# Kernel optimization log

Hardware: AMD Instinct MI355X
Metric: run time of the kernel (lower is better)

The kernel has to match this reference:

```python
import jax, jax.numpy as jnp
import numpy as np

EPS_BN = 1e-5
K_INTERP = 8
K_NEIGH = 16


def _bn(x, g, b):
    # BatchNorm1d in training mode: batch stats over rows (biased var), eps=1e-5
    m = x.mean(axis=0)
    v = x.var(axis=0)
    return (x - m) * jax.lax.rsqrt(v + EPS_BN) * g + b


def _dist(a, b):
    # a:(B,N,3), b:(B,M,3) -> Euclidean distance (B,N,M), computed via the
    # quadratic expansion (clamped at 0) instead of materializing (B,N,M,3)
    d2 = (jnp.sum(a * a, -1)[:, :, None] + jnp.sum(b * b, -1)[:, None, :]
          - 2.0 * jnp.einsum('bnc,bmc->bnm', a, b))
    return jnp.sqrt(jnp.maximum(d2, 0.0))


def _gather(feats, idx):
    # feats:(B,M,C), idx:(B,N,K) int -> (B,N,K,C)
    return jax.vmap(lambda f, i: f[i])(feats, idx)


def setup_inputs() -> dict:
    key = jax.random.key(0)
    B, N1, N2, DS, DD, DOUT = 4, 4096, 1024, 128, 64, 256
    ks = jax.random.split(key, 20)
    s = 0.02
    inp = {
        'p1': jax.random.uniform(ks[0], (B * N1, 3), jnp.float32),
        'x1': jax.random.normal(ks[1], (B * N1, DD), jnp.float32),
        'o1': (jnp.arange(B, dtype=jnp.int32) + 1) * N1,
        'p2': jax.random.uniform(ks[2], (B * N2, 3), jnp.float32),
        'x2': jax.random.normal(ks[3], (B * N2, DS), jnp.float32),
        'o2': (jnp.arange(B, dtype=jnp.int32) + 1) * N2,
        'batch_size': B,
        # dense_mlp: Linear(DD,DS) + BN
        'W_dense': jax.random.normal(ks[4], (DD, DS), jnp.float32) * s,
        'b_dense': jnp.zeros((DS,), jnp.float32),
        'g_dense': jnp.ones((DS,), jnp.float32),
        'bt_dense': jnp.zeros((DS,), jnp.float32),
        # CrossAttentionPointTransformerLayer (dim=DS, hidden_mult=1)
        'Wq': jax.random.normal(ks[5], (DS, DS), jnp.float32) * s,
        'Wk': jax.random.normal(ks[6], (DS, DS), jnp.float32) * s,
        'Wv': jax.random.normal(ks[7], (DS, DS), jnp.float32) * s,
        'W1': jax.random.normal(ks[8], (DS, DS), jnp.float32) * s,
        'b1': jnp.zeros((DS,), jnp.float32),
        'g1': jnp.ones((DS,), jnp.float32),
        'bt1': jnp.zeros((DS,), jnp.float32),
        'W2': jax.random.normal(ks[9], (DS, DS), jnp.float32) * s,
        'b2': jnp.zeros((DS,), jnp.float32),
        # output mlp: Linear(DS+DD, DOUT) + BN
        'W_out': jax.random.normal(ks[10], (DS + DD, DOUT), jnp.float32) * s,
        'b_out': jnp.zeros((DOUT,), jnp.float32),
        'g_out': jnp.ones((DOUT,), jnp.float32),
        'bt_out': jnp.zeros((DOUT,), jnp.float32),
    }
    return inp


def reference(p1, x1, o1, p2, x2, o2, batch_size,
              W_dense, b_dense, g_dense, bt_dense,
              Wq, Wk, Wv, W1, b1, g1, bt1, W2, b2,
              W_out, b_out, g_out, bt_out):
    B = int(batch_size)
    N1 = p1.shape[0] // B
    N2 = p2.shape[0] // B
    DS = x2.shape[-1]

    # dense_mlp
    x1_dense = jax.nn.relu(_bn(x1 @ W_dense + b_dense, g_dense, bt_dense))  # (B*N1, DS)

    # pointops.interpolation(p2, p1, x2, o2, o1, k=8): inverse-distance kNN interp
    p1b = p1.reshape(B, N1, 3)
    p2b = p2.reshape(B, N2, 3)
    x2b = x2.reshape(B, N2, DS)
    d12 = _dist(p1b, p2b)                       # (B,N1,N2)
    negd, idx = jax.lax.top_k(-d12, K_INTERP)   # k nearest in p2
    dknn = -negd
    recip = 1.0 / (dknn + 1e-8)
    w = recip / recip.sum(-1, keepdims=True)    # (B,N1,8)
    x2_interp = jnp.einsum('bnk,bnkc->bnc', w, _gather(x2b, idx))  # (B,N1,DS)

    # CrossAttentionPointTransformerLayer(x_e=x1_dense, x_r=x_d=x2_interp, pos=p1)
    x_e = x1_dense.reshape(B, N1, DS)
    q = x_e @ Wq
    k = x2_interp @ Wk
    v = x2_interp @ Wv
    rel_dist = _dist(p1b, p1b)                  # (B,N1,N1)
    _, nidx = jax.lax.top_k(-rel_dist, K_NEIGH) # 16 nearest neighbors
    kg = _gather(k, nidx)                        # (B,N1,16,DS)
    vg = _gather(v, nidx)
    xeg = _gather(x_e, nidx)
    qk_rel = q[:, :, None, :] - kg
    v2 = vg + xeg
    h = (qk_rel + xeg).reshape(-1, DS)           # (B*N1*16, DS)
    h = jax.nn.relu(_bn(h @ W1 + b1, g1, bt1))
    sim = (h @ W2 + b2).reshape(B, N1, K_NEIGH, DS)
    attn = jax.nn.softmax(sim, axis=-2)          # over neighbors
    agg = jnp.einsum('bnkc,bnkc->bnc', attn, v2).reshape(B * N1, DS)

    # output mlp
    x = jax.nn.relu(_bn(jnp.concatenate([agg, x1], axis=-1) @ W_out + b_out,
                        g_out, bt_out))
    return (p1, x, o1)
```

## Files before the change

kernel.cpp:

```cpp
#include <hip/hip_runtime.h>
#include <math.h>

#define BB 4
#define NN1 4096
#define NN2 1024
#define DS 128
#define DD 64
#define DOUT 256
#define M1 16384
#define MH 262144
#define KCAT 192
#define KI 8
#define KN 16

#define OUT_P1 49152
#define OUT_X  49152
#define OUT_O1 4243456


static const size_t OFF_HPRE = 0;
static const size_t OFF_WTS  = 16777216;
static const size_t OFF_TMP  = 33554432;
static const size_t OFF_XD   = OFF_TMP  + 2097152;
static const size_t OFF_XI   = OFF_XD   + 2097152;
static const size_t OFF_Q    = OFF_XI   + 2097152;
static const size_t OFF_K    = OFF_Q    + 2097152;
static const size_t OFF_V    = OFF_K    + 2097152;
static const size_t OFF_OUTP = OFF_V    + 2097152;
static const size_t OFF_NIDX = OFF_OUTP + 4194304;
static const size_t OFF_STAT = OFF_NIDX + 262144;
static const size_t OFF_P1Q  = OFF_STAT + 4096;
static const size_t OFF_P2Q  = OFF_P1Q  + 65536;
static const size_t OFF_P1S  = OFF_P2Q  + 16384;
static const size_t OFF_P2S  = OFF_P1S  + 65536;

#define WDH 0
#define WDL 8192
#define WQH 16384
#define WQL 32768
#define WKH 49152
#define WKL 65536
#define WVH 81920
#define WVL 98304
#define W1H 114688
#define W1L 131072
#define W2H 147456
#define W2L 163840
#define WOH 180224
#define WOL 229376

typedef __attribute__((ext_vector_type(8))) short short8;
typedef __attribute__((ext_vector_type(4))) float floatx4;
typedef __attribute__((ext_vector_type(2))) float float2v;

__device__ inline unsigned short f2bf(float f) {
    union { float f; unsigned int u; } x; x.f = f;
    unsigned int r = x.u + 0x7fffu + ((x.u >> 16) & 1u);
    return (unsigned short)(r >> 16);
}
__device__ inline float bf2f(unsigned short h) {
    union { unsigned int u; float f; } x; x.u = ((unsigned int)h) << 16;
    return x.f;
}
__device__ inline unsigned long long shfl_xor_u64(unsigned long long v, int m) {
    unsigned lo = (unsigned)v, hi = (unsigned)(v >> 32);
    lo = (unsigned)__shfl_xor((int)lo, m);
    hi = (unsigned)__shfl_xor((int)hi, m);
    return ((unsigned long long)hi << 32) | lo;
}
__device__ inline unsigned cvt_pk_bf16(float lo, float hi) {
    unsigned r;
    asm volatile("v_cvt_pk_bf16_f32 %0, %1, %2" : "=v"(r) : "v"(lo), "v"(hi));
    return r;
}

#define PRO_STAT  (OUT_P1 + BB)
#define PRO_PACK  (PRO_STAT + 3072)
#define PRO_TOTAL (PRO_PACK + M1 + BB*NN2)
#define NPRO 285
struct SwzParams {
    const float* W[7];
    unsigned short* hi[7];
    unsigned short* lo[7];
    int N[7];
    int fid0[8];
};
__global__ __launch_bounds__(256) void k_prolog(
    const float* __restrict__ p1, const int* __restrict__ o1,
    const float* __restrict__ p2, float* __restrict__ out,
    float* __restrict__ stat, float4* __restrict__ p1q,
    float4* __restrict__ p2q, float* __restrict__ p1s,
    float* __restrict__ p2s, SwzParams p)
{
    if (blockIdx.x < NPRO) {
        int i = blockIdx.x * 256 + threadIdx.x;
        if (i < OUT_P1) out[i] = p1[i];
        else if (i < PRO_STAT) out[OUT_O1 + (i - OUT_P1)] = (float)o1[i - OUT_P1];
        else if (i < PRO_PACK) stat[i - PRO_STAT] = 0.f;
        else if (i < PRO_TOTAL) {
            int j = i - PRO_PACK;
            const float* src; float4* dst; float* ps; int jj;
            if (j < M1) { src = p1; dst = p1q; ps = p1s; jj = j; }
            else        { src = p2; dst = p2q; ps = p2s; jj = j - M1; }
            float x = src[jj*3+0] * 16384.f;
            float y = src[jj*3+1] * 16384.f;
            float z = src[jj*3+2] * 16384.f;
            float n = fmaf(z, z, fmaf(y, y, x*x));
            dst[jj] = make_float4(x, y, z, n);
            int pb8 = (jj >> 1)*8 + (jj & 1);
            ps[pb8]   = x; ps[pb8+2] = y;
            ps[pb8+4] = z; ps[pb8+6] = n;
        }
        return;
    }
    int fid = (blockIdx.x - NPRO)*4 + (threadIdx.x >> 6);
    int lane = threadIdx.x & 63;
    if (fid >= 272) return;
    int seg = 0;
    #pragma unroll
    for (int i = 1; i < 7; i++) if (fid >= p.fid0[i]) seg = i;
    int f = fid - p.fid0[seg];
    const float* W = p.W[seg];
    int N = p.N[seg];
    int ncj = N >> 4;
    int slab = f / ncj, cj = f - slab*ncj;
    int n  = cj*16 + (lane & 15);
    int k0 = slab*32 + (lane >> 4)*8;
    unsigned int oh[8], ol[8];
    #pragma unroll
    for (int j = 0; j < 8; j++) {
        float v = W[(size_t)(k0 + j) * N + n];
        unsigned short h = f2bf(v);
        oh[j] = h;
        ol[j] = f2bf(v - bf2f(h));
    }
    uint4 ph, pl;
    ph.x = oh[0] | (oh[1] << 16); ph.y = oh[2] | (oh[3] << 16);
    ph.z = oh[4] | (oh[5] << 16); ph.w = oh[6] | (oh[7] << 16);
    pl.x = ol[0] | (ol[1] << 16); pl.y = ol[2] | (ol[3] << 16);
    pl.z = ol[4] | (ol[5] << 16); pl.w = ol[6] | (ol[7] << 16);
    ((uint4*)p.hi[seg])[f*64 + lane] = ph;
    ((uint4*)p.lo[seg])[f*64 + lane] = pl;
}

template<int N, int K, int MODE, int STATS, int BNA>
__global__ __launch_bounds__(256) void k_gemm_mf(
    const float* __restrict__ Amat, const unsigned short* __restrict__ Whi,
    const unsigned short* __restrict__ Wlo, const float* __restrict__ bias,
    float* __restrict__ C, const float* __restrict__ aux,
    float* __restrict__ sums, float* __restrict__ sumsq,
    const float* __restrict__ bsums, const float* __restrict__ bsumsq,
    const float* __restrict__ bg, const float* __restrict__ bbt)
{
    __shared__ float sstat[STATS ? 2*N : 1];
    __shared__ float sbn[BNA ? 2*DS : 1];
    const int t = threadIdx.x, w = t >> 6, lane = t & 63;
    const int quad = lane >> 4, c = lane & 15;
    const int row = blockIdx.x*64 + w*16 + c;
    const int sA = (MODE == 2) ? DS : K;
    constexpr int nslab = K >> 5;
    constexpr int ncj = N >> 4;
    const int seg = (MODE == 3) ? blockIdx.y : 0;
    const float* Abase = (MODE == 3 && seg > 0) ? aux : Amat;
    const unsigned short* WhiS = Whi + (size_t)seg*32768;
    const unsigned short* WloS = Wlo + (size_t)seg*32768;
    float* CS = C + (size_t)seg*2097152;
    unsigned short* CS16 = (unsigned short*)C + (size_t)seg*4194304;
    if (STATS) {
        for (int i = t; i < 2*N; i += 256) sstat[i] = 0.f;
    }
    if (BNA) {
        if (t < DS) {
            const float invM = 1.f / (float)M1;
            float m   = bsums[t] * invM;
            float var = bsumsq[t] * invM - m*m;
            float sc  = bg[t] * rsqrtf(var + 1e-5f);
            sbn[t] = sc;
            sbn[DS + t] = bbt[t] - m * sc;
        }
    }
    if (STATS || BNA) __syncthreads();

    floatx4 acc[ncj];
    #pragma unroll
    for (int cj = 0; cj < ncj; cj++) acc[cj] = (floatx4){0.f,0.f,0.f,0.f};

    #pragma unroll
    for (int slab = 0; slab < nslab; slab++) {
        const int kk = slab*32 + quad*8;
        const float* src;
        if (MODE == 2 && kk >= DS) src = aux + (size_t)row*DD + (kk - DS);
        else                       src = Abase + (size_t)row*sA + kk;
        floatx4 va = *(const floatx4*)src;
        floatx4 vb = *(const floatx4*)(src + 4);
        if (BNA && MODE == 3 && seg == 0) {
            #pragma unroll
            for (int j = 0; j < 4; j++) {
                va[j] = fmaxf(fmaf(va[j], sbn[kk+j],   sbn[DS+kk+j]),   0.f);
                vb[j] = fmaxf(fmaf(vb[j], sbn[kk+4+j], sbn[DS+kk+4+j]), 0.f);
            }
        }
        short8 ahi, alo;
        #pragma unroll
        for (int j = 0; j < 4; j++) {
            unsigned short h = f2bf(va[j]);
            ahi[j] = (short)h; alo[j] = (short)f2bf(va[j] - bf2f(h));
        }
        #pragma unroll
        for (int j = 0; j < 4; j++) {
            unsigned short h = f2bf(vb[j]);
            ahi[4+j] = (short)h; alo[4+j] = (short)f2bf(vb[j] - bf2f(h));
        }
        const short8* bh = (const short8*)WhiS + (size_t)slab*ncj*64;
        const short8* bl = (const short8*)WloS + (size_t)slab*ncj*64;
        #pragma unroll
        for (int cj = 0; cj < ncj; cj++) {
            short8 bhv = bh[cj*64 + lane];
            short8 blv = bl[cj*64 + lane];
            acc[cj] = __builtin_amdgcn_mfma_f32_16x16x32_bf16(alo, bhv, acc[cj], 0, 0, 0);
            acc[cj] = __builtin_amdgcn_mfma_f32_16x16x32_bf16(ahi, blv, acc[cj], 0, 0, 0);
            acc[cj] = __builtin_amdgcn_mfma_f32_16x16x32_bf16(ahi, bhv, acc[cj], 0, 0, 0);
        }
    }
    const int rbase = blockIdx.x*64 + w*16 + quad*4;
    #pragma unroll
    for (int cj = 0; cj < ncj; cj++) {
        const float bb = bias ? bias[cj*16 + c] : 0.f;
        float s = 0.f, ss = 0.f;
        #pragma unroll
        for (int p = 0; p < 4; p++) {
            float v = acc[cj][p] + bb;
            if (MODE == 3) {
                if (seg > 0) {
                    float xv = Amat[(size_t)(rbase + p)*DS + cj*16 + c];
                    if (BNA) xv = fmaxf(fmaf(xv, sbn[cj*16+c], sbn[DS+cj*16+c]), 0.f);
                    if (seg == 1) v = xv - v;
                    else          v += xv;
                }
                CS16[(size_t)(rbase + p)*N + cj*16 + c] = f2bf(v);
            } else {
                CS[(size_t)(rbase + p)*N + cj*16 + c] = v;
            }
            if (STATS) { s += v; ss += v*v; }
        }
        if (STATS) {
            s  += __shfl_xor(s, 16);  s  += __shfl_xor(s, 32);
            ss += __shfl_xor(ss, 16); ss += __shfl_xor(ss, 32);
            if (quad == 0) {
                atomicAdd(&sstat[cj*16 + c], s);
                atomicAdd(&sstat[N + cj*16 + c], ss);
            }
        }
    }
    if (STATS) {
        __syncthreads();
        for (int i = t; i < N; i += 256) {
            atomicAdd(&sums[i],  sstat[i]);
            atomicAdd(&sumsq[i], sstat[N + i]);
        }
    }
}

__global__ __launch_bounds__(256) void k_gemm_qe(
    const unsigned short* __restrict__ q16, const unsigned short* __restrict__ e16,
    const unsigned short* __restrict__ W1hi, const float* __restrict__ b1,
    float* __restrict__ qw, float* __restrict__ ew)
{
    const int t = threadIdx.x, w = t >> 6, lane = t & 63;
    const int quad = lane >> 4, c = lane & 15;
    const int y = blockIdx.y;
    const unsigned short* A = y ? e16 : q16;
    float* C = y ? ew : qw;
    const int row = blockIdx.x*64 + w*16 + c;

    floatx4 acc[8];
    #pragma unroll
    for (int cj = 0; cj < 8; cj++) acc[cj] = (floatx4){0.f,0.f,0.f,0.f};

    #pragma unroll
    for (int slab = 0; slab < 4; slab++) {
        uint4 av = *(const uint4*)(A + (size_t)row*DS + slab*32 + quad*8);
        short8 af;
        ((uint4*)&af)[0] = av;
        const short8* bh = (const short8*)W1hi + (size_t)slab*8*64;
        #pragma unroll
        for (int cj = 0; cj < 8; cj++) {
            short8 bhv = bh[cj*64 + lane];
            acc[cj] = __builtin_amdgcn_mfma_f32_16x16x32_bf16(af, bhv, acc[cj], 0, 0, 0);
        }
    }
    const int rbase = blockIdx.x*64 + w*16 + quad*4;
    #pragma unroll
    for (int cj = 0; cj < 8; cj++) {
        const float bb = y ? b1[cj*16 + c] : 0.f;
        #pragma unroll
        for (int p = 0; p < 4; p++)
            C[(size_t)(rbase + p)*DS + cj*16 + c] = acc[cj][p] + bb;
    }
}

__global__ __launch_bounds__(256) void k_hadd(
    const float* __restrict__ qw, const float* __restrict__ ew,
    const int* __restrict__ nidx, unsigned short* __restrict__ hpre,
    float* __restrict__ sums, float* __restrict__ sumsq)
{
    __shared__ float sstat[256];
    const int t = threadIdx.x, w = t >> 6, lane = t & 63;
    sstat[t] = 0.f;
    __syncthreads();
    const int rr = lane & 7, cg = lane >> 3;
    const int wr0 = blockIdx.x*128 + w*32;
    const int cb = cg*16;

    float sv[16], sq[16];
    #pragma unroll
    for (int j = 0; j < 16; j++) { sv[j] = 0.f; sq[j] = 0.f; }

    #pragma unroll
    for (int p = 0; p < 4; p++) {
        const int r = wr0 + p*8 + rr;
        const int i = r >> 4;
        const int m = nidx[r];
        const float4* Ap = (const float4*)(qw + (size_t)i*DS + cb);
        const float4* Bp = (const float4*)(ew + (size_t)m*DS + cb);
        float4 a0 = Ap[0], a1 = Ap[1], a2 = Ap[2], a3 = Ap[3];
        float4 b0 = Bp[0], b1v = Bp[1], b2 = Bp[2], b3 = Bp[3];
        float v[16];
        v[0]=a0.x+b0.x;  v[1]=a0.y+b0.y;  v[2]=a0.z+b0.z;  v[3]=a0.w+b0.w;
        v[4]=a1.x+b1v.x; v[5]=a1.y+b1v.y; v[6]=a1.z+b1v.z; v[7]=a1.w+b1v.w;
        v[8]=a2.x+b2.x;  v[9]=a2.y+b2.y;  v[10]=a2.z+b2.z; v[11]=a2.w+b2.w;
        v[12]=a3.x+b3.x; v[13]=a3.y+b3.y; v[14]=a3.z+b3.z; v[15]=a3.w+b3.w;
        #pragma unroll
        for (int j = 0; j < 16; j++) { sv[j] += v[j]; sq[j] = fmaf(v[j], v[j], sq[j]); }
        uint4 pk0, pk1;
        pk0.x = cvt_pk_bf16(v[0],  v[1]);  pk0.y = cvt_pk_bf16(v[2],  v[3]);
        pk0.z = cvt_pk_bf16(v[4],  v[5]);  pk0.w = cvt_pk_bf16(v[6],  v[7]);
        pk1.x = cvt_pk_bf16(v[8],  v[9]);  pk1.y = cvt_pk_bf16(v[10], v[11]);
        pk1.z = cvt_pk_bf16(v[12], v[13]); pk1.w = cvt_pk_bf16(v[14], v[15]);
        uint4* dst = (uint4*)(hpre + (size_t)r*DS + cb);
        dst[0] = pk0; dst[1] = pk1;
    }
    #pragma unroll
    for (int m2 = 1; m2 < 8; m2 <<= 1) {
        #pragma unroll
        for (int j = 0; j < 16; j++) {
            sv[j] += __shfl_xor(sv[j], m2);
            sq[j] += __shfl_xor(sq[j], m2);
        }
    }
    if (rr == 0) {
        #pragma unroll
        for (int j = 0; j < 16; j++) {
            atomicAdd(&sstat[cb + j], sv[j]);
            atomicAdd(&sstat[128 + cb + j], sq[j]);
        }
    }
    __syncthreads();
    if (t < 128) atomicAdd(&sums[t], sstat[t]);
    else         atomicAdd(&sumsq[t - 128], sstat[t]);
}

__global__ __launch_bounds__(256) void k_attn2(
    const unsigned short* __restrict__ hpre, const float* __restrict__ sums_h,
    const float* __restrict__ sumsq_h, const float* __restrict__ g1,
    const float* __restrict__ bt1, const unsigned short* __restrict__ W2sw,
    const unsigned short* __restrict__ v, const int* __restrict__ nidx,
    float* __restrict__ agg)
{
    __shared__ unsigned short WF[16384];
    __shared__ float s_sc[DS], s_sh[DS];
    const int t = threadIdx.x;
    #pragma unroll
    for (int i = 0; i < 8; i++)
        ((uint4*)WF)[t + 256*i] = ((const uint4*)W2sw)[t + 256*i];
    if (t < DS) {
        const float invM = 1.f / (float)MH;
        float m   = sums_h[t] * invM;
        float var = sumsq_h[t] * invM - m*m;
        float sc  = g1[t] * rsqrtf(var + 1e-5f);
        s_sc[t] = sc;
        s_sh[t] = bt1[t] - m * sc;
    }
    __syncthreads();

    const int w = t >> 6, lane = t & 63;
    const int gp = blockIdx.x * 4 + w;
    const int quad = lane >> 4, c = lane & 15;

    floatx4 acc[8];
    #pragma unroll
    for (int cj = 0; cj < 8; cj++) acc[cj] = (floatx4){0.f, 0.f, 0.f, 0.f};

    for (int ks = 0; ks < 4; ks++) {
        const int ko = ks*32 + quad*8;
        const unsigned short* hp = hpre + ((size_t)gp*16 + c)*DS + ko;
        uint4 hv = *(const uint4*)hp;
        floatx4 sc0 = *(const floatx4*)&s_sc[ko];
        floatx4 sc1 = *(const floatx4*)&s_sc[ko + 4];
        floatx4 sh0 = *(const floatx4*)&s_sh[ko];
        floatx4 sh1 = *(const floatx4*)&s_sh[ko + 4];
        unsigned int hw[4] = {hv.x, hv.y, hv.z, hv.w};
        short8 af;
        #pragma unroll
        for (int j = 0; j < 4; j++) {
            unsigned short u0 = (unsigned short)(hw[j] & 0xffffu);
            unsigned short u1 = (unsigned short)(hw[j] >> 16);
            float f0 = fmaxf(fmaf(bf2f(u0), (j<2)?sc0[2*j]:sc1[2*j-4],   (j<2)?sh0[2*j]:sh1[2*j-4]),   0.f);
            float f1 = fmaxf(fmaf(bf2f(u1), (j<2)?sc0[2*j+1]:sc1[2*j-3], (j<2)?sh0[2*j+1]:sh1[2*j-3]), 0.f);
            af[2*j]   = (short)f2bf(f0);
            af[2*j+1] = (short)f2bf(f1);
        }
        #pragma unroll
        for (int cj = 0; cj < 8; cj++) {
            short8 bfv = ((const short8*)WF)[(ks*8 + cj)*64 + lane];
            acc[cj] = __builtin_amdgcn_mfma_f32_16x16x32_bf16(af, bfv, acc[cj], 0, 0, 0);
        }
    }

    int nid[4];
    #pragma unroll
    for (int p = 0; p < 4; p++) nid[p] = nidx[gp*16 + quad*4 + p];

    #pragma unroll
    for (int cj = 0; cj < 8; cj++) {
        float m4 = fmaxf(fmaxf(acc[cj][0], acc[cj][1]), fmaxf(acc[cj][2], acc[cj][3]));
        m4 = fmaxf(m4, __shfl_xor(m4, 16));
        m4 = fmaxf(m4, __shfl_xor(m4, 32));
        float e[4]; float s4 = 0.f;
        #pragma unroll
        for (int p = 0; p < 4; p++) { e[p] = __expf(acc[cj][p] - m4); s4 += e[p]; }
        s4 += __shfl_xor(s4, 16); s4 += __shfl_xor(s4, 32);
        const float inv = 1.f / s4;
        const int col = cj*16 + c;
        float a = 0.f;
        #pragma unroll
        for (int p = 0; p < 4; p++)
            a = fmaf(e[p]*inv, bf2f(v[(size_t)nid[p]*DS + col]), a);
        a += __shfl_xor(a, 16); a += __shfl_xor(a, 32);
        if (quad == 0) agg[(size_t)gp*DS + col] = a;
    }
}

__global__ __launch_bounds__(256) void k_bnrelu(
    const float4* __restrict__ X, const float* __restrict__ sums,
    const float* __restrict__ sumsq, const float* __restrict__ g,
    const float* __restrict__ bt, float invM,
    float4* __restrict__ Y, size_t total4, int N)
{
    size_t i = (size_t)blockIdx.x * 256 + threadIdx.x;
    if (i < total4) {
        int c = (int)((i*4) & (size_t)(N - 1));
        float4 sm = *(const float4*)(sums + c);
        float4 sq = *(const float4*)(sumsq + c);
        float4 gg = *(const float4*)(g + c);
        float4 bb = *(const float4*)(bt + c);
        float4 x = X[i], y;
        float m0 = sm.x*invM, m1 = sm.y*invM, m2 = sm.z*invM, m3 = sm.w*invM;
        float s0 = gg.x*rsqrtf(sq.x*invM - m0*m0 + 1e-5f);
        float s1 = gg.y*rsqrtf(sq.y*invM - m1*m1 + 1e-5f);
        float s2 = gg.z*rsqrtf(sq.z*invM - m2*m2 + 1e-5f);
        float s3 = gg.w*rsqrtf(sq.w*invM - m3*m3 + 1e-5f);
        y.x = fmaxf(fmaf(x.x, s0, bb.x - m0*s0), 0.f);
        y.y = fmaxf(fmaf(x.y, s1, bb.y - m1*s1), 0.f);
        y.z = fmaxf(fmaf(x.z, s2, bb.z - m2*s2), 0.f);
        y.w = fmaxf(fmaf(x.w, s3, bb.w - m3*s3), 0.f);
        Y[i] = y;
    }
}

template<int NCAND, int KSEL, int EPI, int CAP>
__device__ __forceinline__ void sel_body(
    int gp0,
    const float4* __restrict__ qpts4, const float4* __restrict__ cpts4,
    const float* __restrict__ cpairs,
    int* __restrict__ nidx, const float* __restrict__ x2, float* __restrict__ xi,
    unsigned* hist0, unsigned* hist1,
    unsigned* skey, unsigned* sidx,
    float* swtE, unsigned* sidxE,
    unsigned* wpart, int* sstate)
{
    const int b = gp0 >> 12;
    const int t = threadIdx.x, wv = t >> 6, lane = t & 63;
    constexpr int ITER  = NCAND / 256;
    constexpr int PITER = NCAND / 512;

    const float4 qv0 = qpts4[gp0];
    const float4 qv1 = qpts4[gp0 + 1];
    const float4* pb = cpts4 + (size_t)b*NCAND;
    const float*  pbs = cpairs + (size_t)b*NCAND*4;

    unsigned kreg[2][ITER];
    if (t < 16)      ((uint4*)hist0)[t]      = (uint4){0u,0u,0u,0u};
    else if (t < 32) ((uint4*)hist1)[t - 16] = (uint4){0u,0u,0u,0u};
    __syncthreads();

    {
        const float2v qx0 = {qv0.x, qv0.x}, qy0 = {qv0.y, qv0.y};
        const float2v qz0 = {qv0.z, qv0.z}, qw0 = {qv0.w, qv0.w};
        const float2v qx1 = {qv1.x, qv1.x}, qy1 = {qv1.y, qv1.y};
        const float2v qz1 = {qv1.z, qv1.z}, qw1 = {qv1.w, qv1.w};
        const float2v m2 = {-2.f, -2.f}, z2 = {0.f, 0.f};
        #pragma unroll
        for (int pi = 0; pi < PITER; pi++) {
            const int ip = t + 256*pi;
            float4 A  = ((const float4*)pbs)[2*ip];
            float4 Bv = ((const float4*)pbs)[2*ip + 1];
            float2v xp = {A.x, A.y},  yp = {A.z, A.w};
            float2v zp = {Bv.x, Bv.y}, wp = {Bv.z, Bv.w};
            float2v t0 = __builtin_elementwise_fma(yp, qy0, xp*qx0);
            t0 = __builtin_elementwise_fma(zp, qz0, t0);
            float2v d0 = __builtin_elementwise_fma(t0, m2, wp + qw0);
            d0 = __builtin_elementwise_max(d0, z2);
            float2v t1 = __builtin_elementwise_fma(yp, qy1, xp*qx1);
            t1 = __builtin_elementwise_fma(zp, qz1, t1);
            float2v d1 = __builtin_elementwise_fma(t1, m2, wp + qw1);
            d1 = __builtin_elementwise_max(d1, z2);
            unsigned ka = (unsigned)d0[0], kb = (unsigned)d0[1];
            unsigned kc = (unsigned)d1[0], kd = (unsigned)d1[1];
            kreg[0][2*pi] = ka; kreg[0][2*pi+1] = kb;
            kreg[1][2*pi] = kc; kreg[1][2*pi+1] = kd;
            if ((ka >> 20) < CAP) atomicAdd(&hist0[ka >> 20], 1u);
            if ((kb >> 20) < CAP) atomicAdd(&hist0[kb >> 20], 1u);
            if ((kc >> 20) < CAP) atomicAdd(&hist1[kc >> 20], 1u);
            if ((kd >> 20) < CAP) atomicAdd(&hist1[kd >> 20], 1u);
        }
    }
    __syncthreads();

    if (wv < 2) {
        unsigned* H = wv ? hist1 : hist0;
        unsigned h = (lane < CAP) ? H[lane] : 0u;
        unsigned incl = h;
        #pragma unroll
        for (int off = 1; off < 64; off <<= 1) {
            unsigned o = (unsigned)__shfl_up((int)incl, off);
            if (lane >= off) incl += o;
        }
        unsigned excl = incl - h;
        const int base = wv*8;
        if ((int)excl < KSEL && KSEL <= (int)(excl + h)) {
            sstate[base+0] = lane; sstate[base+1] = (int)excl; sstate[base+2] = (int)h;
            sstate[base+3] = ((int)(excl + h) <= 64) ? 1 : 0;
            sstate[base+4] = 0;
        }
        unsigned tot = (unsigned)__shfl((int)incl, 63);
        if (lane == 0 && (int)tot < KSEL) sstate[base+3] = -1;
    }
    __syncthreads();

    if (sstate[3] == -1 || sstate[11] == -1) {
        for (int qi = 0; qi < 2; qi++) {
            if (sstate[qi*8+3] != -1) continue;
            ((uint4*)hist0)[t] = (uint4){0u,0u,0u,0u};
            __syncthreads();
            #pragma unroll
            for (int it = 0; it < ITER; it++)
                atomicAdd(&hist0[kreg[qi][it] >> 20], 1u);
            __syncthreads();
            uint4 h4 = ((const uint4*)hist0)[t];
            unsigned hv[4] = {h4.x, h4.y, h4.z, h4.w};
            unsigned tsum = hv[0]+hv[1]+hv[2]+hv[3];
            unsigned incl = tsum;
            #pragma unroll
            for (int off = 1; off < 64; off <<= 1) {
                unsigned o = (unsigned)__shfl_up((int)incl, off);
                if (lane >= off) incl += o;
            }
            if (lane == 63) wpart[wv] = incl;
            __syncthreads();
            unsigned wbase = 0;
            for (int i2 = 0; i2 < wv; i2++) wbase += wpart[i2];
            unsigned excl = wbase + incl - tsum;
            if ((int)excl < KSEL && KSEL <= (int)(excl + tsum)) {
                unsigned cum = excl;
                #pragma unroll
                for (int i2 = 0; i2 < 4; i2++) {
                    unsigned h = hv[i2];
                    if ((int)cum < KSEL && KSEL <= (int)(cum + h)) {
                        sstate[qi*8+0] = t*4 + i2; sstate[qi*8+1] = (int)cum;
                        sstate[qi*8+2] = (int)h;
                        sstate[qi*8+3] = ((int)cum + (int)h <= 64) ? 1 : 0;
                        sstate[qi*8+4] = 0;
                        break;
                    }
                    cum += h;
                }
            }
            __syncthreads();
        }
    }

    if (sstate[3] == 1 && sstate[11] == 1) {
        const unsigned P0 = (unsigned)sstate[0];
        const unsigned P1 = (unsigned)sstate[8];
        #pragma unroll
        for (int pi = 0; pi < PITER; pi++) {
            const int ip = t + 256*pi;
            #pragma unroll
            for (int c2 = 0; c2 < 2; c2++) {
                const int j = 2*ip + c2;
                const unsigned k0 = kreg[0][2*pi+c2], k1 = kreg[1][2*pi+c2];
                if ((k0 >> 20) <= P0) {
                    int pos = (int)atomicAdd((unsigned*)&sstate[4], 1u);
                    skey[pos] = k0; sidx[pos] = (unsigned)j;
                }
                if ((k1 >> 20) <= P1) {
                    int pos = (int)atomicAdd((unsigned*)&sstate[12], 1u);
                    skey[64 + pos] = k1; sidx[64 + pos] = (unsigned)j;
                }
            }
        }
    } else {
        #pragma unroll
        for (int qi = 0; qi < 2; qi++) {
            const float4 qv = qi ? qv1 : qv0;
            unsigned P = (unsigned)sstate[qi*8+0];
            int S = sstate[qi*8+1], cntB = sstate[qi*8+2], mode = sstate[qi*8+3];
            int gsh = 20;
            if (mode == 0) {
                for (int round = 1; round < 4; round++) {
                    const int nb  = (round == 3) ? 16 : 256;
                    const int wb  = (round == 3) ? 4 : 8;
                    const int sh  = (round == 1) ? 12 : (round == 2 ? 4 : 0);
                    const int psh = sh + wb;
                    if (t < nb) hist0[t] = 0u;
                    __syncthreads();
                    #pragma unroll
                    for (int it = 0; it < ITER; it++) {
                        unsigned key = kreg[qi][it];
                        if ((key >> psh) == P)
                            atomicAdd(&hist0[(key >> sh) & (nb - 1)], 1u);
                    }
                    __syncthreads();
                    unsigned hv = (t < nb) ? hist0[t] : 0u;
                    unsigned tsum = hv;
                    unsigned incl = tsum;
                    #pragma unroll
                    for (int off = 1; off < 64; off <<= 1) {
                        unsigned o = (unsigned)__shfl_up((int)incl, off);
                        if (lane >= off) incl += o;
                    }
                    if (lane == 63) wpart[wv] = incl;
                    __syncthreads();
                    unsigned wbase = 0;
                    for (int i2 = 0; i2 < wv; i2++) wbase += wpart[i2];
                    unsigned exclT = wbase + incl - tsum;
                    const int need = KSEL - S;
                    if ((int)exclT < need && need <= (int)(exclT + tsum)) {
                        int Snew = S + (int)exclT;
                        int tot  = Snew + (int)tsum;
                        sstate[qi*8+0] = (int)((P << wb) | (unsigned)t);
                        sstate[qi*8+1] = Snew; sstate[qi*8+2] = (int)tsum;
                        sstate[qi*8+3] = (tot <= 64) ? 1 : ((round == 3) ? 2 : 0);
                        sstate[qi*8+4] = 0;
                    }
                    __syncthreads();
                    P = (unsigned)sstate[qi*8+0]; S = sstate[qi*8+1];
                    cntB = sstate[qi*8+2]; mode = sstate[qi*8+3];
                    gsh = sh;
                    if (mode) break;
                }
            }
            if (mode == 1) {
                #pragma unroll
                for (int pi = 0; pi < PITER; pi++) {
                    const int ip = t + 256*pi;
                    #pragma unroll
                    for (int c2 = 0; c2 < 2; c2++) {
                        const int j = 2*ip + c2;
                        unsigned key = kreg[qi][2*pi+c2];
                        if ((key >> gsh) <= P) {
                            int pos = (int)atomicAdd((unsigned*)&sstate[qi*8+4], 1u);
                            skey[qi*64 + pos] = key; sidx[qi*64 + pos] = (unsigned)j;
                        }
                    }
                }
            } else if (mode != 1) {
                if (t < 64) {
                    const unsigned long long lmask = (1ull << lane) - 1ull;
                    int cnt = 0;
                    for (int pass = 0; pass < 2; pass++) {
                        for (int it = 0; it < NCAND/64; it++) {
                            int j = lane + 64*it;
                            float4 cv = pb[j];
                            float dot = fmaf(qv.z, cv.z, fmaf(qv.y, cv.y, qv.x*cv.x));
                            float d2 = fmaxf(fmaf(-2.f, dot, qv.w + cv.w), 0.f);
                            unsigned key = (unsigned)d2;
                            bool f = pass ? (key == P) : (key < P);
                            unsigned long long bal = __ballot(f);
                            if (f) {
                                int pos = cnt + __popcll(bal & lmask);
                                if (pos < 64) { skey[qi*64 + pos] = key; sidx[qi*64 + pos] = (unsigned)j; }
                            }
                            cnt += __popcll(bal);
                        }
                    }
                    if (lane == 0) { sstate[qi*8+1] = min(cnt, 64); sstate[qi*8+2] = 0; }
                }
            }
            __syncthreads();
        }
    }
    __syncthreads();

    if (wv < 2) {
        const int q = wv;
        const int total = sstate[q*8+1] + sstate[q*8+2];
        unsigned long long v = ~0ull;
        if (lane < total)
            v = (((unsigned long long)skey[q*64 + lane]) << 32) | sidx[q*64 + lane];
        #pragma unroll
        for (int k = 2; k <= 64; k <<= 1) {
            #pragma unroll
            for (int jj = k >> 1; jj > 0; jj >>= 1) {
                unsigned long long p = shfl_xor_u64(v, jj);
                bool up = ((lane & k) == 0);
                bool takeMin = (((lane & jj) == 0) == up);
                bool pl = p < v;
                v = (takeMin == pl) ? p : v;
            }
        }
        if (EPI == 0) {
            if (lane < KSEL)
                nidx[(gp0 + q)*KSEL + lane] = b*NCAND + (int)(v & 0xffffffffull);
        } else {
            const float4 qq = q ? qv1 : qv0;
            float wgt = 0.f;
            unsigned si = (unsigned)(v & 0xffffffffull);
            if (lane < KSEL) {
                float4 cv = pb[si];
                float dot = fmaf(qq.z, cv.z, fmaf(qq.y, cv.y, qq.x*cv.x));
                float d2 = fmaxf(fmaf(-2.f, dot, qq.w + cv.w), 0.f);
                wgt = 1.f / (sqrtf(d2) + 1.6384e-4f);
            }
            float ws = wgt;
            ws += __shfl_xor(ws, 1); ws += __shfl_xor(ws, 2); ws += __shfl_xor(ws, 4);
            if (lane < KSEL) {
                swtE[q*KSEL + lane]  = wgt / ws;
                sidxE[q*KSEL + lane] = si;
            }
        }
    }

    if (EPI == 1) {
        __syncthreads();
        const int qi2 = t >> 7, tt = t & 127;
        const float* x2b = x2 + (size_t)b*NCAND*DS;
        float a = 0.f;
        #pragma unroll
        for (int r = 0; r < KSEL; r++)
            a = fmaf(swtE[qi2*KSEL + r], x2b[(size_t)sidxE[qi2*KSEL + r]*DS + tt], a);
        xi[(size_t)(gp0 + qi2)*DS + tt] = a;
    }
}

__global__ __launch_bounds__(256) void k_sel2(
    const float4* __restrict__ p1q, const float4* __restrict__ p2q,
    const float* __restrict__ p1s, const float* __restrict__ p2s,
    int* __restrict__ nidx, const float* __restrict__ x2, float* __restrict__ xi)
{
    __shared__ __align__(16) unsigned hist0[1024], hist1[1024];
    __shared__ __align__(16) unsigned skey[128], sidx[128];
    __shared__ float    swtE[2*KI];
    __shared__ unsigned sidxE[2*KI];
    __shared__ unsigned wpart[8];
    __shared__ int      sstate[20];
    const int bid = blockIdx.x;
    if (bid < M1/2) {
        sel_body<NN1, KN, 0, 32>(bid*2, p1q, p1q, p1s, nidx, nullptr, nullptr,
                                 hist0, hist1, skey, sidx, swtE, sidxE, wpart, sstate);
    } else {
        sel_body<NN2, KI, 1, 64>((bid - M1/2)*2, p1q, p2q, p2s, nullptr, x2, xi,
                                 hist0, hist1, skey, sidx, swtE, sidxE, wpart, sstate);
    }
}

extern "C" void kernel_launch(void* const* d_in, const int* in_sizes, int n_in,
                              void* d_out, int out_size, void* d_ws, size_t ws_size,
                              hipStream_t stream)
{
    const float* p1 = (const float*)d_in[0];
    const float* x1 = (const float*)d_in[1];
    const int*   o1 = (const int*)d_in[2];
    const float* p2 = (const float*)d_in[3];
    const float* x2 = (const float*)d_in[4];
    const float* W_dense = (const float*)d_in[7];
    const float* b_dense = (const float*)d_in[8];
    const float* g_dense = (const float*)d_in[9];
    const float* bt_dense= (const float*)d_in[10];
    const float* Wq = (const float*)d_in[11];
    const float* Wk = (const float*)d_in[12];
    const float* Wv = (const float*)d_in[13];
    const float* W1 = (const float*)d_in[14];
    const float* b1 = (const float*)d_in[15];
    const float* g1 = (const float*)d_in[16];
    const float* bt1= (const float*)d_in[17];
    const float* W2 = (const float*)d_in[18];
    const float* W_out = (const float*)d_in[20];
    const float* b_out = (const float*)d_in[21];
    const float* g_out = (const float*)d_in[22];
    const float* bt_out= (const float*)d_in[23];

    float* ws   = (float*)d_ws;
    unsigned short* hpre = (unsigned short*)(ws + OFF_HPRE);
    unsigned short* wts  = (unsigned short*)(ws + OFF_WTS);
    float* tmp  = ws + OFF_TMP;
    float* qw1f = ws + OFF_XD;
    float* ew1f = ws + OFF_OUTP;
    float* xi   = ws + OFF_XI;
    float* qm   = ws + OFF_Q;
    float* outp = ws + OFF_OUTP;
    int*   nidx = (int*)(ws + OFF_NIDX);
    float* stat = ws + OFF_STAT;
    float4* p1q = (float4*)(ws + OFF_P1Q);
    float4* p2q = (float4*)(ws + OFF_P2Q);
    float* p1s = ws + OFF_P1S;
    float* p2s = ws + OFF_P2S;
    unsigned short* q16 = (unsigned short*)(ws + OFF_Q);
    unsigned short* e16 = (unsigned short*)(ws + OFF_K);
    unsigned short* v16 = (unsigned short*)(ws + OFF_V);
    float* sums_d = stat,      *sumsq_d = stat+256;
    float* sums_h = stat+1024, *sumsq_h = stat+1280;
    float* sums_o = stat+2048, *sumsq_o = stat+2304;
    float* out = (float*)d_out;

    SwzParams sp;
    sp.W[0]=W_dense; sp.W[1]=Wq; sp.W[2]=Wk; sp.W[3]=Wv; sp.W[4]=W1; sp.W[5]=W2; sp.W[6]=W_out;
    sp.hi[0]=wts+WDH; sp.hi[1]=wts+WQH; sp.hi[2]=wts+WKH; sp.hi[3]=wts+WVH;
    sp.hi[4]=wts+W1H; sp.hi[5]=wts+W2H; sp.hi[6]=wts+WOH;
    sp.lo[0]=wts+WDL; sp.lo[1]=wts+WQL; sp.lo[2]=wts+WKL; sp.lo[3]=wts+WVL;
    sp.lo[4]=wts+W1L; sp.lo[5]=wts+W2L; sp.lo[6]=wts+WOL;
    sp.N[0]=128; sp.N[1]=128; sp.N[2]=128; sp.N[3]=128; sp.N[4]=128; sp.N[5]=128; sp.N[6]=256;
    sp.fid0[0]=0; sp.fid0[1]=16; sp.fid0[2]=48; sp.fid0[3]=80; sp.fid0[4]=112;
    sp.fid0[5]=144; sp.fid0[6]=176; sp.fid0[7]=272;
    k_prolog<<<NPRO + 68, 256, 0, stream>>>(p1, o1, p2, out, stat, p1q, p2q, p1s, p2s, sp);

    k_sel2<<<M1, 256, 0, stream>>>(p1q, p2q, p1s, p2s, nidx, x2, xi);

    k_gemm_mf<128,64,0,1,0><<<M1/64, 256, 0, stream>>>(x1, wts+WDH, wts+WDL, b_dense, tmp,
        nullptr, sums_d, sumsq_d, nullptr, nullptr, nullptr, nullptr);

    k_gemm_mf<128,128,3,0,1><<<dim3(M1/64,3), 256, 0, stream>>>(tmp, wts+WQH, wts+WQL,
        nullptr, qm, xi, nullptr, nullptr, sums_d, sumsq_d, g_dense, bt_dense);

    k_gemm_qe<<<dim3(M1/64, 2), 256, 0, stream>>>(q16, e16, wts+W1H, b1, qw1f, ew1f);
    k_hadd<<<MH/128, 256, 0, stream>>>(qw1f, ew1f, nidx, hpre, sums_h, sumsq_h);

    k_attn2<<<M1/4, 256, 0, stream>>>(hpre, sums_h, sumsq_h, g1, bt1, wts+W2H, v16, nidx, tmp);

    k_gemm_mf<256,192,2,1,0><<<M1/64, 256, 0, stream>>>(tmp, wts+WOH, wts+WOL, b_out, outp,
        x1, sums_o, sumsq_o, nullptr, nullptr, nullptr, nullptr);
    k_bnrelu<<<(M1*DOUT/4)/256, 256, 0, stream>>>((const float4*)outp, sums_o, sumsq_o,
        g_out, bt_out, 1.f/(float)M1, (float4*)(out + OUT_X), (size_t)M1*DOUT/4, DOUT);
}
```

Baseline: 342.3 us.

## Drop materialized bf16 hpre buffer; recompute q+e in attention, factor BN stats

```diff
diff --git a/kernel.cpp b/kernel.cpp
--- a/kernel.cpp
+++ b/kernel.cpp
@@ -108,8 +108,8 @@
             float n = fmaf(z, z, fmaf(y, y, x*x));
             dst[jj] = make_float4(x, y, z, n);
             int pb8 = (jj >> 1)*8 + (jj & 1);
-            ps[pb8]   = x; ps[pb8+2] = y;
-            ps[pb8+4] = z; ps[pb8+6] = n;
+            ps[pb8]   = x + x; ps[pb8+2] = y + y;
+            ps[pb8+4] = z + z; ps[pb8+6] = n;
         }
         return;
     }
@@ -299,71 +299,47 @@
     }
 }
 
-__global__ __launch_bounds__(256) void k_hadd(
+__global__ __launch_bounds__(256) void k_hstat(
     const float* __restrict__ qw, const float* __restrict__ ew,
-    const int* __restrict__ nidx, unsigned short* __restrict__ hpre,
+    const int* __restrict__ nidx,
     float* __restrict__ sums, float* __restrict__ sumsq)
 {
     __shared__ float sstat[256];
     const int t = threadIdx.x, w = t >> 6, lane = t & 63;
     sstat[t] = 0.f;
     __syncthreads();
-    const int rr = lane & 7, cg = lane >> 3;
-    const int wr0 = blockIdx.x*128 + w*32;
-    const int cb = cg*16;
-
-    float sv[16], sq[16];
-    #pragma unroll
-    for (int j = 0; j < 16; j++) { sv[j] = 0.f; sq[j] = 0.f; }
-
-    #pragma unroll
-    for (int p = 0; p < 4; p++) {
-        const int r = wr0 + p*8 + rr;
-        const int i = r >> 4;
-        const int m = nidx[r];
-        const float4* Ap = (const float4*)(qw + (size_t)i*DS + cb);
-        const float4* Bp = (const float4*)(ew + (size_t)m*DS + cb);
-        float4 a0 = Ap[0], a1 = Ap[1], a2 = Ap[2], a3 = Ap[3];
-        float4 b0 = Bp[0], b1v = Bp[1], b2 = Bp[2], b3 = Bp[3];
-        float v[16];
-        v[0]=a0.x+b0.x;  v[1]=a0.y+b0.y;  v[2]=a0.z+b0.z;  v[3]=a0.w+b0.w;
-        v[4]=a1.x+b1v.x; v[5]=a1.y+b1v.y; v[6]=a1.z+b1v.z; v[7]=a1.w+b1v.w;
-        v[8]=a2.x+b2.x;  v[9]=a2.y+b2.y;  v[10]=a2.z+b2.z; v[11]=a2.w+b2.w;
-        v[12]=a3.x+b3.x; v[13]=a3.y+b3.y; v[14]=a3.z+b3.z; v[15]=a3.w+b3.w;
-        #pragma unroll
-        for (int j = 0; j < 16; j++) { sv[j] += v[j]; sq[j] = fmaf(v[j], v[j], sq[j]); }
-        uint4 pk0, pk1;
-        pk0.x = cvt_pk_bf16(v[0],  v[1]);  pk0.y = cvt_pk_bf16(v[2],  v[3]);
-        pk0.z = cvt_pk_bf16(v[4],  v[5]);  pk0.w = cvt_pk_bf16(v[6],  v[7]);
-        pk1.x = cvt_pk_bf16(v[8],  v[9]);  pk1.y = cvt_pk_bf16(v[10], v[11]);
-        pk1.z = cvt_pk_bf16(v[12], v[13]); pk1.w = cvt_pk_bf16(v[14], v[15]);
-        uint4* dst = (uint4*)(hpre + (size_t)r*DS + cb);
-        dst[0] = pk0; dst[1] = pk1;
-    }
-    #pragma unroll
-    for (int m2 = 1; m2 < 8; m2 <<= 1) {
-        #pragma unroll
-        for (int j = 0; j < 16; j++) {
-            sv[j] += __shfl_xor(sv[j], m2);
-            sq[j] += __shfl_xor(sq[j], m2);
-        }
-    }
-    if (rr == 0) {
-        #pragma unroll
-        for (int j = 0; j < 16; j++) {
-            atomicAdd(&sstat[cb + j], sv[j]);
-            atomicAdd(&sstat[128 + cb + j], sq[j]);
-        }
-    }
+    const int col = lane*2;
+    float Sx = 0.f, Sy = 0.f, SSx = 0.f, SSy = 0.f;
+    #pragma unroll
+    for (int g2 = 0; g2 < 4; g2++) {
+        const int gp = blockIdx.x*16 + w*4 + g2;
+        float2 a = *(const float2*)(qw + (size_t)gp*DS + col);
+        float B1x = 0.f, B1y = 0.f, B2x = 0.f, B2y = 0.f;
+        const int* np = nidx + gp*16;
+        #pragma unroll
+        for (int cc = 0; cc < 16; cc++) {
+            int m = np[cc];
+            float2 b = *(const float2*)(ew + (size_t)m*DS + col);
+            B1x += b.x; B1y += b.y;
+            B2x = fmaf(b.x, b.x, B2x); B2y = fmaf(b.y, b.y, B2y);
+        }
+        Sx += fmaf(16.f, a.x, B1x);
+        Sy += fmaf(16.f, a.y, B1y);
+        SSx += fmaf(16.f*a.x, a.x, fmaf(2.f*a.x, B1x, B2x));
+        SSy += fmaf(16.f*a.y, a.y, fmaf(2.f*a.y, B1y, B2y));
+    }
+    atomicAdd(&sstat[col],       Sx); atomicAdd(&sstat[col+1],       Sy);
+    atomicAdd(&sstat[128 + col], SSx); atomicAdd(&sstat[128 + col+1], SSy);
     __syncthreads();
     if (t < 128) atomicAdd(&sums[t], sstat[t]);
     else         atomicAdd(&sumsq[t - 128], sstat[t]);
 }
 
-__global__ __launch_bounds__(256) void k_attn2(
-    const unsigned short* __restrict__ hpre, const float* __restrict__ sums_h,
-    const float* __restrict__ sumsq_h, const float* __restrict__ g1,
-    const float* __restrict__ bt1, const unsigned short* __restrict__ W2sw,
+__global__ __launch_bounds__(256) void k_attn3(
+    const float* __restrict__ qw, const float* __restrict__ ew,
+    const float* __restrict__ sums_h, const float* __restrict__ sumsq_h,
+    const float* __restrict__ g1, const float* __restrict__ bt1,
+    const unsigned short* __restrict__ W2sw,
     const unsigned short* __restrict__ v, const int* __restrict__ nidx,
     float* __restrict__ agg)
 {
@@ -386,6 +362,7 @@
     const int w = t >> 6, lane = t & 63;
     const int gp = blockIdx.x * 4 + w;
     const int quad = lane >> 4, c = lane & 15;
+    const int mrow = nidx[gp*16 + c];
 
     floatx4 acc[8];
     #pragma unroll
@@ -393,23 +370,26 @@
 
     for (int ks = 0; ks < 4; ks++) {
         const int ko = ks*32 + quad*8;
-        const unsigned short* hp = hpre + ((size_t)gp*16 + c)*DS + ko;
-        uint4 hv = *(const uint4*)hp;
+        const float* qp = qw + (size_t)gp*DS + ko;
+        const float* ep = ew + (size_t)mrow*DS + ko;
+        floatx4 qa = *(const floatx4*)qp;
+        floatx4 qb = *(const floatx4*)(qp + 4);
+        floatx4 ea = *(const floatx4*)ep;
+        floatx4 eb = *(const floatx4*)(ep + 4);
         floatx4 sc0 = *(const floatx4*)&s_sc[ko];
         floatx4 sc1 = *(const floatx4*)&s_sc[ko + 4];
         floatx4 sh0 = *(const floatx4*)&s_sh[ko];
         floatx4 sh1 = *(const floatx4*)&s_sh[ko + 4];
-        unsigned int hw[4] = {hv.x, hv.y, hv.z, hv.w};
+        float f[8];
+        #pragma unroll
+        for (int j = 0; j < 4; j++) {
+            f[j]   = fmaxf(fmaf(qa[j] + ea[j], sc0[j], sh0[j]), 0.f);
+            f[4+j] = fmaxf(fmaf(qb[j] + eb[j], sc1[j], sh1[j]), 0.f);
+        }
         short8 af;
         #pragma unroll
-        for (int j = 0; j < 4; j++) {
-            unsigned short u0 = (unsigned short)(hw[j] & 0xffffu);
-            unsigned short u1 = (unsigned short)(hw[j] >> 16);
-            float f0 = fmaxf(fmaf(bf2f(u0), (j<2)?sc0[2*j]:sc1[2*j-4],   (j<2)?sh0[2*j]:sh1[2*j-4]),   0.f);
-            float f1 = fmaxf(fmaf(bf2f(u1), (j<2)?sc0[2*j+1]:sc1[2*j-3], (j<2)?sh0[2*j+1]:sh1[2*j-3]), 0.f);
-            af[2*j]   = (short)f2bf(f0);
-            af[2*j+1] = (short)f2bf(f1);
-        }
+        for (int j = 0; j < 4; j++)
+            ((unsigned*)&af)[j] = cvt_pk_bf16(f[2*j], f[2*j+1]);
         #pragma unroll
         for (int cj = 0; cj < 8; cj++) {
             short8 bfv = ((const short8*)WF)[(ks*8 + cj)*64 + lane];
@@ -495,11 +475,10 @@
     __syncthreads();
 
     {
-        const float2v qx0 = {qv0.x, qv0.x}, qy0 = {qv0.y, qv0.y};
-        const float2v qz0 = {qv0.z, qv0.z}, qw0 = {qv0.w, qv0.w};
-        const float2v qx1 = {qv1.x, qv1.x}, qy1 = {qv1.y, qv1.y};
-        const float2v qz1 = {qv1.z, qv1.z}, qw1 = {qv1.w, qv1.w};
-        const float2v m2 = {-2.f, -2.f}, z2 = {0.f, 0.f};
+        const float2v nqx0 = {-qv0.x, -qv0.x}, nqy0 = {-qv0.y, -qv0.y};
+        const float2v nqz0 = {-qv0.z, -qv0.z}, qw0 = {qv0.w, qv0.w};
+        const float2v nqx1 = {-qv1.x, -qv1.x}, nqy1 = {-qv1.y, -qv1.y};
+        const float2v nqz1 = {-qv1.z, -qv1.z}, qw1 = {qv1.w, qv1.w};
         #pragma unroll
         for (int pi = 0; pi < PITER; pi++) {
             const int ip = t + 256*pi;
@@ -507,14 +486,14 @@
             float4 Bv = ((const float4*)pbs)[2*ip + 1];
             float2v xp = {A.x, A.y},  yp = {A.z, A.w};
             float2v zp = {Bv.x, Bv.y}, wp = {Bv.z, Bv.w};
-            float2v t0 = __builtin_elementwise_fma(yp, qy0, xp*qx0);
-            t0 = __builtin_elementwise_fma(zp, qz0, t0);
-            float2v d0 = __builtin_elementwise_fma(t0, m2, wp + qw0);
-            d0 = __builtin_elementwise_max(d0, z2);
-            float2v t1 = __builtin_elementwise_fma(yp, qy1, xp*qx1);
-            t1 = __builtin_elementwise_fma(zp, qz1, t1);
-            float2v d1 = __builtin_elementwise_fma(t1, m2, wp + qw1);
-            d1 = __builtin_elementwise_max(d1, z2);
+            float2v d0 = wp + qw0;
+            d0 = __builtin_elementwise_fma(xp, nqx0, d0);
+            d0 = __builtin_elementwise_fma(yp, nqy0, d0);
+            d0 = __builtin_elementwise_fma(zp, nqz0, d0);
+            float2v d1 = wp + qw1;
+            d1 = __builtin_elementwise_fma(xp, nqx1, d1);
+            d1 = __builtin_elementwise_fma(yp, nqy1, d1);
+            d1 = __builtin_elementwise_fma(zp, nqz1, d1);
             unsigned ka = (unsigned)d0[0], kb = (unsigned)d0[1];
             unsigned kc = (unsigned)d1[0], kd = (unsigned)d1[1];
             kreg[0][2*pi] = ka; kreg[0][2*pi+1] = kb;
@@ -802,7 +781,6 @@
     const float* bt_out= (const float*)d_in[23];
 
     float* ws   = (float*)d_ws;
-    unsigned short* hpre = (unsigned short*)(ws + OFF_HPRE);
     unsigned short* wts  = (unsigned short*)(ws + OFF_WTS);
     float* tmp  = ws + OFF_TMP;
     float* qw1f = ws + OFF_XD;
@@ -844,9 +822,10 @@
         nullptr, qm, xi, nullptr, nullptr, sums_d, sumsq_d, g_dense, bt_dense);
 
     k_gemm_qe<<<dim3(M1/64, 2), 256, 0, stream>>>(q16, e16, wts+W1H, b1, qw1f, ew1f);
-    k_hadd<<<MH/128, 256, 0, stream>>>(qw1f, ew1f, nidx, hpre, sums_h, sumsq_h);
-
-    k_attn2<<<M1/4, 256, 0, stream>>>(hpre, sums_h, sumsq_h, g1, bt1, wts+W2H, v16, nidx, tmp);
+    k_hstat<<<M1/16, 256, 0, stream>>>(qw1f, ew1f, nidx, sums_h, sumsq_h);
+
+    k_attn3<<<M1/4, 256, 0, stream>>>(qw1f, ew1f, sums_h, sumsq_h, g1, bt1,
+        wts+W2H, v16, nidx, tmp);
 
     k_gemm_mf<256,192,2,1,0><<<M1/64, 256, 0, stream>>>(tmp, wts+WOH, wts+WOL, b_out, outp,
         x1, sums_o, sumsq_o, nullptr, nullptr, nullptr, nullptr);
```

Result: faster. 322.0 us (-5.9%).
